# Performance work log

Hardware: AMD Instinct MI355X
Metric: run time of the kernel (lower is better)

## Reference

```python
import jax, jax.numpy as jnp
import numpy as np

N = 20000   # nodes
E = 320000  # edges (avg degree 16)
F = 8       # n_original_features (tokens per node)
D = 16      # embed_dim
H = 4       # num_heads
OUT = 7     # classes


def setup_inputs() -> dict:
    key = jax.random.key(0)
    ks = jax.random.split(key, 12)
    s = 0.1
    return {
        "x": jax.random.normal(ks[0], (N, F * D), dtype=jnp.float32),
        "edge_index": jax.random.randint(ks[1], (2, E), 0, N, dtype=jnp.int32),
        "conv1_wqkv": jax.random.normal(ks[2], (3 * D, D), dtype=jnp.float32) * s,
        "conv1_bqkv": jnp.zeros((3 * D,), dtype=jnp.float32),
        "conv1_wo": jax.random.normal(ks[3], (D, D), dtype=jnp.float32) * s,
        "conv1_bo": jnp.zeros((D,), dtype=jnp.float32),
        "conv2_wqkv": jax.random.normal(ks[4], (3 * D, D), dtype=jnp.float32) * s,
        "conv2_bqkv": jnp.zeros((3 * D,), dtype=jnp.float32),
        "conv2_wo": jax.random.normal(ks[5], (D, D), dtype=jnp.float32) * s,
        "conv2_bo": jnp.zeros((D,), dtype=jnp.float32),
        "out_w": jax.random.normal(ks[6], (OUT, F * D), dtype=jnp.float32) * s,
        "out_b": jnp.zeros((OUT,), dtype=jnp.float32),
    }


def _mha_edge(xq, xkv, wqkv, bqkv, wo, bo):
    # xq, xkv: [E, F, D]. torch MultiheadAttention: query=xq, key=value=xkv.
    dh = D // H
    wq, wk, wv = jnp.split(wqkv, 3, axis=0)
    bq, bk, bv = jnp.split(bqkv, 3)
    q = (xq @ wq.T + bq).reshape(-1, F, H, dh)
    k = (xkv @ wk.T + bk).reshape(-1, F, H, dh)
    v = (xkv @ wv.T + bv).reshape(-1, F, H, dh)
    scale = 1.0 / np.sqrt(dh).astype(np.float32)
    scores = jnp.einsum('efhd,eghd->ehfg', q, k) * scale  # [E,H,F,F]
    attn = jax.nn.softmax(scores, axis=-1)
    out = jnp.einsum('ehfg,eghd->efhd', attn, v).reshape(-1, F, D)
    return out @ wo.T + bo


def _amp_conv(x, src, dst, wqkv, bqkv, wo, bo):
    # gather per-edge token views; query = target node tokens (x_i), key/value = source (x_j)
    xj = x[src].reshape(-1, F, D)
    xi = x[dst].reshape(-1, F, D)
    msg = _mha_edge(xi, xj, wqkv, bqkv, wo, bo).reshape(-1, F * D)
    return jax.ops.segment_sum(msg, dst, num_segments=N)  # aggr='add' at targets


def reference(x, edge_index, conv1_wqkv, conv1_bqkv, conv1_wo, conv1_bo,
              conv2_wqkv, conv2_bqkv, conv2_wo, conv2_bo, out_w, out_b):
    src, dst = edge_index[0], edge_index[1]
    h = _amp_conv(x, src, dst, conv1_wqkv, conv1_bqkv, conv1_wo, conv1_bo)
    h = jax.nn.elu(h)
    h = _amp_conv(h, src, dst, conv2_wqkv, conv2_bqkv, conv2_wo, conv2_bo)
    h = jax.nn.elu(h)
    logits = h @ out_w.T + out_b
    return jax.nn.log_softmax(logits, axis=1)
```

## Files before the change

### kernel.cpp

```cpp
#include <hip/hip_runtime.h>
#include <hip/hip_bf16.h>
#include <math.h>

#define NN 20000
#define NE 320000
#define FT 8
#define DM 16
#define FD 128
#define OUTC 7
#define CHK 20
#define DEGB 1250

typedef unsigned short ushort;
typedef unsigned int uint;
typedef __fp16 h2 __attribute__((ext_vector_type(2)));
union UH { uint u; h2 h; };

__device__ inline h2 u2h(uint x) { UH c; c.u = x; return c.h; }

__device__ inline float dot2(uint a, h2 b, float c) {
#if __has_builtin(__builtin_amdgcn_fdot2)
    return __builtin_amdgcn_fdot2(u2h(a), b, c, false);
#else
    h2 ah = u2h(a);
    return fmaf((float)ah.x, (float)b.x, fmaf((float)ah.y, (float)b.y, c));
#endif
}
__device__ inline float dot2u(uint a, uint b, float c) { return dot2(a, u2h(b), c); }
__device__ inline float dot2h(h2 a, h2 b, float c) {
#if __has_builtin(__builtin_amdgcn_fdot2)
    return __builtin_amdgcn_fdot2(a, b, c, false);
#else
    return fmaf((float)a.x, (float)b.x, fmaf((float)a.y, (float)b.y, c));
#endif
}

__device__ inline h2 pk(float a, float b) {
#if __has_builtin(__builtin_amdgcn_cvt_pkrtz)
    return __builtin_amdgcn_cvt_pkrtz(a, b);
#else
    h2 r; r.x = (__fp16)a; r.y = (__fp16)b; return r;
#endif
}
__device__ inline ushort f16b(float x) {
    union { __fp16 h; ushort u; } c; c.h = (__fp16)x; return c.u;
}
__device__ inline float rcpf(float x) {
#if __has_builtin(__builtin_amdgcn_rcpf)
    return __builtin_amdgcn_rcpf(x);
#else
    return 1.0f / x;
#endif
}
__device__ inline float exp2r(float x) {
#if __has_builtin(__builtin_amdgcn_exp2f)
    return __builtin_amdgcn_exp2f(x);
#else
    return exp2f(x);
#endif
}
__device__ inline float elu_f(float x) {
    return x > 0.f ? x : exp2r(x * 1.4426950408889634f) - 1.0f;
}

__device__ inline void wave_lds_fence() { __threadfence_block(); }

#define QSCALE 0.7213475204444817f


__global__ __launch_bounds__(256) void qkv1_deg_kernel(
    const float* __restrict__ x,
    const float* __restrict__ wqkv, const float* __restrict__ bqkv,
    const int* __restrict__ dst, int* __restrict__ deg,
    ushort* __restrict__ qout, ushort* __restrict__ kvout) {
    if (blockIdx.x < DEGB) {
        const int e = blockIdx.x * 256 + threadIdx.x;
        if (e < NE) atomicAdd(&deg[dst[e]], 1);
        return;
    }
    __shared__ float sw[48 * 17];
    __shared__ float sb[48];
    __shared__ float sx[2][FD];
    __shared__ uint squ[2][64];
    __shared__ uint skvu[2][128];
    const int t = threadIdx.x;
    const int nh = t >> 7, tl = t & 127;
    const int nbase = (blockIdx.x - DEGB) * 4;
    for (int i = t; i < 48 * 16; i += 256) sw[(i >> 4) * 17 + (i & 15)] = wqkv[i];
    if (t < 48) sb[t] = bqkv[t];
    const int f = tl >> 4, d = tl & 15, h = d >> 2, dd = d & 3;
#pragma unroll
    for (int it = 0; it < 2; ++it) {
        const int n = nbase + it * 2 + nh;
        if (it) __syncthreads();
        sx[nh][tl] = x[(size_t)n * FD + tl];
        __syncthreads();
        float aq = sb[d], ak = sb[16 + d], av = sb[32 + d];
        const float* xr = &sx[nh][f * 16];
#pragma unroll
        for (int e = 0; e < 16; ++e) {
            const float xe = xr[e];
            aq = fmaf(xe, sw[d * 17 + e], aq);
            ak = fmaf(xe, sw[(16 + d) * 17 + e], ak);
            av = fmaf(xe, sw[(32 + d) * 17 + e], av);
        }
        ushort* sq = (ushort*)squ[nh];
        ushort* skv = (ushort*)skvu[nh];
        sq[tl] = f16b(aq * QSCALE);
        skv[h * 64 + f * 4 + dd] = f16b(ak);
        skv[h * 64 + 32 + dd * 8 + f] = f16b(av);
        __syncthreads();
        if (tl < 64) ((uint*)(qout + (size_t)n * FD))[tl] = squ[nh][tl];
        ((uint*)(kvout + (size_t)n * 256))[tl] = skvu[nh][tl];
    }
}

__global__ __launch_bounds__(1024) void scan_kernel(const int* __restrict__ deg,
                                                    int* __restrict__ rowstart,
                                                    int* __restrict__ cursor) {
    __shared__ int wsum[16];
    const int t = threadIdx.x;
    const int lane = t & 63, wid = t >> 6;
    const int base = t * CHK;
    int local[CHK];
    int s = 0;
#pragma unroll
    for (int i = 0; i < CHK; ++i) {
        const int idx = base + i;
        const int d = (idx < NN) ? deg[idx] : 0;
        local[i] = s;
        s += d;
    }
    int ws = s;
    for (int off = 1; off < 64; off <<= 1) {
        int tmp = __shfl_up(ws, off);
        if (lane >= off) ws += tmp;
    }
    if (lane == 63) wsum[wid] = ws;
    __syncthreads();
    if (wid == 0) {
        int v = (lane < 16) ? wsum[lane] : 0;
        for (int off = 1; off < 16; off <<= 1) {
            int tmp = __shfl_up(v, off);
            if (lane >= off) v += tmp;
        }
        if (lane < 16) wsum[lane] = v;
    }
    __syncthreads();
    const int excl = (ws - s) + (wid > 0 ? wsum[wid - 1] : 0);
#pragma unroll
    for (int i = 0; i < CHK; ++i) {
        const int idx = base + i;
        if (idx < NN) {
            const int v = excl + local[i];
            rowstart[idx] = v;
            cursor[idx] = v;
        }
    }
    if (t == 0) rowstart[NN] = NE;
}

__global__ __launch_bounds__(256) void scatter_kernel(
    const int* __restrict__ src, const int* __restrict__ dst,
    int* __restrict__ cursor, int* __restrict__ csr_src) {
    const int e = blockIdx.x * 256 + threadIdx.x;
    if (e < NE) {
        const int pos = atomicAdd(&cursor[dst[e]], 1);
        csr_src[pos] = src[e];
    }
}

template <int PHASE>
__global__ __launch_bounds__(256) void edge_fused_kernel(
    const int* __restrict__ rowstart, const int* __restrict__ csr_src,
    const ushort* __restrict__ qh, const uint* __restrict__ kvw,
    const float* __restrict__ wo, const float* __restrict__ bo,
    const float* __restrict__ w2, const float* __restrict__ b2,
    ushort* __restrict__ qout, ushort* __restrict__ kvout,
    float* __restrict__ out) {
    __shared__ float swb[1200];
    __shared__ float srow[4][FD];
    __shared__ uint spack[4][192];
    const int t = threadIdx.x;
    for (int i = t; i < 256; i += 256) swb[(i >> 4) * 17 + (i & 15)] = wo[i];
    if (t < 16) swb[272 + t] = bo[t];
    if (PHASE == 1) {
        for (int i = t; i < 768; i += 256) swb[288 + (i >> 4) * 17 + (i & 15)] = w2[i];
        if (t < 48) swb[1104 + t] = b2[t];
    } else {
        for (int i = t; i < OUTC * FD; i += 256) swb[288 + i] = w2[i];
        if (t < OUTC) swb[1184 + t] = b2[t];
    }
    __syncthreads();

    const int wv = t >> 6;
    const int n = blockIdx.x * 4 + wv;
    const int lane = t & 63;
    const int slot = lane >> 2, h = lane & 3;
    const h2 one2 = {(__fp16)1.0f, (__fp16)1.0f};

    const uint* qrow = (const uint*)(qh + (size_t)n * FD);
    uint2 qp[8];
#pragma unroll
    for (int f = 0; f < 8; ++f)
        qp[f] = *(const uint2*)(qrow + f * 8 + h * 2);

    const int beg = rowstart[n], end = rowstart[n + 1];

    float acc[8][4];
#pragma unroll
    for (int f = 0; f < 8; ++f)
#pragma unroll
        for (int dd = 0; dd < 4; ++dd) acc[f][dd] = 0.f;

    int e = beg + slot;
    uint idx = (e < end) ? (uint)csr_src[e] : 0u;
    float gate = (e < end) ? 1.0f : 0.0f;

    for (int eb = beg; eb < end; eb += 16) {
        const uint4* p = (const uint4*)(kvw + (size_t)idx * 128 + h * 32);
        const uint4 k0 = p[0], k1 = p[1], k2 = p[2], k3 = p[3];
        const uint4 v0 = p[4], v1 = p[5], v2 = p[6], v3 = p[7];
        const int en = eb + 16 + slot;
        const uint idxn = (en < end) ? (uint)csr_src[en] : 0u;
        const float gaten = (en < end) ? 1.0f : 0.0f;

#pragma unroll
        for (int f = 0; f < 8; ++f) {
            const uint qx = qp[f].x, qy = qp[f].y;
            float s0 = dot2u(qy, k0.y, dot2u(qx, k0.x, 0.f));
            float s1 = dot2u(qy, k0.w, dot2u(qx, k0.z, 0.f));
            float s2 = dot2u(qy, k1.y, dot2u(qx, k1.x, 0.f));
            float s3 = dot2u(qy, k1.w, dot2u(qx, k1.z, 0.f));
            float s4 = dot2u(qy, k2.y, dot2u(qx, k2.x, 0.f));
            float s5 = dot2u(qy, k2.w, dot2u(qx, k2.z, 0.f));
            float s6 = dot2u(qy, k3.y, dot2u(qx, k3.x, 0.f));
            float s7 = dot2u(qy, k3.w, dot2u(qx, k3.z, 0.f));
            s0 = exp2r(s0); s1 = exp2r(s1); s2 = exp2r(s2); s3 = exp2r(s3);
            s4 = exp2r(s4); s5 = exp2r(s5); s6 = exp2r(s6); s7 = exp2r(s7);
            const h2 e0 = pk(s0, s1), e1 = pk(s2, s3), e2 = pk(s4, s5), e3 = pk(s6, s7);
            const float sum =
                dot2h(e3, one2, dot2h(e2, one2, dot2h(e1, one2, dot2h(e0, one2, 0.f))));
            const float inv = gate * rcpf(sum);
            const float p0 = dot2(v0.w, e3, dot2(v0.z, e2, dot2(v0.y, e1, dot2(v0.x, e0, 0.f))));
            const float p1 = dot2(v1.w, e3, dot2(v1.z, e2, dot2(v1.y, e1, dot2(v1.x, e0, 0.f))));
            const float p2 = dot2(v2.w, e3, dot2(v2.z, e2, dot2(v2.y, e1, dot2(v2.x, e0, 0.f))));
            const float p3 = dot2(v3.w, e3, dot2(v3.z, e2, dot2(v3.y, e1, dot2(v3.x, e0, 0.f))));
            acc[f][0] = fmaf(p0, inv, acc[f][0]);
            acc[f][1] = fmaf(p1, inv, acc[f][1]);
            acc[f][2] = fmaf(p2, inv, acc[f][2]);
            acc[f][3] = fmaf(p3, inv, acc[f][3]);
        }
        idx = idxn; gate = gaten;
    }

#pragma unroll
    for (int f = 0; f < 8; ++f)
#pragma unroll
        for (int dd = 0; dd < 4; ++dd) {
            float a = acc[f][dd];
            a += __shfl_xor(a, 4);
            a += __shfl_xor(a, 8);
            a += __shfl_xor(a, 16);
            a += __shfl_xor(a, 32);
            acc[f][dd] = a;
        }
    if (slot == 0) {
#pragma unroll
        for (int f = 0; f < 8; ++f)
            *(float4*)(&srow[wv][f * 16 + h * 4]) =
                make_float4(acc[f][0], acc[f][1], acc[f][2], acc[f][3]);
    }
    wave_lds_fence();

    const int dgr = end - beg;
    const int f0 = lane >> 4, d = lane & 15;
    const float* swo = swb;
    const float* sbo = swb + 272;
    float hv0 = (float)dgr * sbo[d];
    float hv1 = hv0;
#pragma unroll
    for (int ee = 0; ee < 16; ++ee) {
        const float wde = swo[d * 17 + ee];
        hv0 = fmaf(srow[wv][f0 * 16 + ee], wde, hv0);
        hv1 = fmaf(srow[wv][(f0 + 4) * 16 + ee], wde, hv1);
    }
    hv0 = elu_f(hv0);
    hv1 = elu_f(hv1);

    if (PHASE == 1) {
        srow[wv][lane] = hv0;
        srow[wv][lane + 64] = hv1;
        wave_lds_fence();
        const float* swq = swb + 288;
        const float* sbq = swb + 1104;
        float aq0 = sbq[d], ak0 = sbq[16 + d], av0 = sbq[32 + d];
        float aq1 = aq0, ak1 = ak0, av1 = av0;
#pragma unroll
        for (int ee = 0; ee < 16; ++ee) {
            const float x0 = srow[wv][f0 * 16 + ee];
            const float x1 = srow[wv][(f0 + 4) * 16 + ee];
            const float wq = swq[d * 17 + ee];
            const float wk = swq[(16 + d) * 17 + ee];
            const float wvw = swq[(32 + d) * 17 + ee];
            aq0 = fmaf(x0, wq, aq0); aq1 = fmaf(x1, wq, aq1);
            ak0 = fmaf(x0, wk, ak0); ak1 = fmaf(x1, wk, ak1);
            av0 = fmaf(x0, wvw, av0); av1 = fmaf(x1, wvw, av1);
        }
        ushort* sq = (ushort*)&spack[wv][0];
        ushort* skv = (ushort*)&spack[wv][64];
        const int hh = d >> 2, dd = d & 3;
        sq[lane] = f16b(aq0 * QSCALE);
        sq[lane + 64] = f16b(aq1 * QSCALE);
        skv[hh * 64 + f0 * 4 + dd] = f16b(ak0);
        skv[hh * 64 + (f0 + 4) * 4 + dd] = f16b(ak1);
        skv[hh * 64 + 32 + dd * 8 + f0] = f16b(av0);
        skv[hh * 64 + 32 + dd * 8 + f0 + 4] = f16b(av1);
        wave_lds_fence();
        ((uint*)(qout + (size_t)n * FD))[lane] = spack[wv][lane];
        uint* kvo = (uint*)(kvout + (size_t)n * 256);
        kvo[lane] = spack[wv][64 + lane];
        kvo[lane + 64] = spack[wv][128 + lane];
    } else {
        const float* scw = swb + 288;
        const float* scb = swb + 1184;
        float p[OUTC];
#pragma unroll
        for (int c = 0; c < OUTC; ++c)
            p[c] = fmaf(hv0, scw[c * FD + lane], hv1 * scw[c * FD + lane + 64]);
#pragma unroll
        for (int c = 0; c < OUTC; ++c)
            for (int off = 32; off; off >>= 1) p[c] += __shfl_xor(p[c], off);
        if (lane == 0) {
            float lg[OUTC];
            float m = -1e30f;
#pragma unroll
            for (int c = 0; c < OUTC; ++c) { lg[c] = p[c] + scb[c]; m = fmaxf(m, lg[c]); }
            float s = 0.f;
#pragma unroll
            for (int c = 0; c < OUTC; ++c) s += __expf(lg[c] - m);
            const float lse = m + logf(s);
#pragma unroll
            for (int c = 0; c < OUTC; ++c) out[(size_t)n * OUTC + c] = lg[c] - lse;
        }
    }
}

extern "C" void kernel_launch(void* const* d_in, const int* in_sizes, int n_in,
                              void* d_out, int out_size, void* d_ws, size_t ws_size,
                              hipStream_t stream) {
    const float* x      = (const float*)d_in[0];
    const int*   ei     = (const int*)d_in[1];
    const float* w1qkv  = (const float*)d_in[2];
    const float* b1qkv  = (const float*)d_in[3];
    const float* w1o    = (const float*)d_in[4];
    const float* b1o    = (const float*)d_in[5];
    const float* w2qkv  = (const float*)d_in[6];
    const float* b2qkv  = (const float*)d_in[7];
    const float* w2o    = (const float*)d_in[8];
    const float* b2o    = (const float*)d_in[9];
    const float* outw   = (const float*)d_in[10];
    const float* outb   = (const float*)d_in[11];
    float* out = (float*)d_out;

    const int* srcp = ei;
    const int* dstp = ei + NE;

    ushort* qh    = (ushort*)d_ws;
    ushort* kvh   = qh + (size_t)NN * FD;
    ushort* qh2   = kvh + (size_t)NN * 256;
    ushort* kvh2  = qh2 + (size_t)NN * FD;
    int*    deg      = (int*)(kvh2 + (size_t)NN * 256);
    int*    rowstart = deg + NN;
    int*    cursor   = rowstart + NN + 1;
    int*    csr_src  = cursor + NN;

    (void)hipMemsetAsync(deg, 0, NN * sizeof(int), stream);
    qkv1_deg_kernel<<<DEGB + NN / 4, 256, 0, stream>>>(x, w1qkv, b1qkv, dstp, deg, qh, kvh);
    scan_kernel<<<1, 1024, 0, stream>>>(deg, rowstart, cursor);
    scatter_kernel<<<(NE + 255) / 256, 256, 0, stream>>>(srcp, dstp, cursor, csr_src);

    edge_fused_kernel<1><<<NN / 4, 256, 0, stream>>>(
        rowstart, csr_src, qh, (const uint*)kvh, w1o, b1o, w2qkv, b2qkv,
        qh2, kvh2, nullptr);
    edge_fused_kernel<2><<<NN / 4, 256, 0, stream>>>(
        rowstart, csr_src, qh2, (const uint*)kvh2, w2o, b2o, outw, outb,
        nullptr, nullptr, out);
}
```

Measured before the change: 204.7 us.

## Split each node's edge loop across two wavefronts and reduce through LDS

Each destination node is now handled by two wavefronts instead of one, each taking alternate chunks of 16 edges, and the grid doubles to NN/2 blocks. Partial accumulators are combined through a second shared-memory row after a block barrier, and the second wave exits early. The aim is to shorten the per-node serial edge loop (average degree 16, so about two chunks) and raise parallelism. The cost is more blocks that each reload weights into LDS, an added __syncthreads, and half the waves sitting idle during the epilogue.

```diff
diff --git a/kernel.cpp b/kernel.cpp
--- a/kernel.cpp
+++ b/kernel.cpp
@@ -179,8 +179,9 @@
     ushort* __restrict__ qout, ushort* __restrict__ kvout,
     float* __restrict__ out) {
     __shared__ float swb[1200];
-    __shared__ float srow[4][FD];
-    __shared__ uint spack[4][192];
+    __shared__ float srow[2][FD];
+    __shared__ float srow2[2][FD];
+    __shared__ uint spack[2][192];
     const int t = threadIdx.x;
     for (int i = t; i < 256; i += 256) swb[(i >> 4) * 17 + (i & 15)] = wo[i];
     if (t < 16) swb[272 + t] = bo[t];
@@ -193,8 +194,10 @@
     }
     __syncthreads();
 
-    const int wv = t >> 6;
-    const int n = blockIdx.x * 4 + wv;
+    const int w4 = t >> 6;
+    const int nh = w4 >> 1;
+    const int ww = w4 & 1;
+    const int n = blockIdx.x * 2 + nh;
     const int lane = t & 63;
     const int slot = lane >> 2, h = lane & 3;
     const h2 one2 = {(__fp16)1.0f, (__fp16)1.0f};
@@ -213,15 +216,16 @@
 #pragma unroll
         for (int dd = 0; dd < 4; ++dd) acc[f][dd] = 0.f;
 
-    int e = beg + slot;
+    const int wbeg = beg + ww * 16;
+    int e = wbeg + slot;
     uint idx = (e < end) ? (uint)csr_src[e] : 0u;
     float gate = (e < end) ? 1.0f : 0.0f;
 
-    for (int eb = beg; eb < end; eb += 16) {
+    for (int eb = wbeg; eb < end; eb += 32) {
         const uint4* p = (const uint4*)(kvw + (size_t)idx * 128 + h * 32);
         const uint4 k0 = p[0], k1 = p[1], k2 = p[2], k3 = p[3];
         const uint4 v0 = p[4], v1 = p[5], v2 = p[6], v3 = p[7];
-        const int en = eb + 16 + slot;
+        const int en = eb + 32 + slot;
         const uint idxn = (en < end) ? (uint)csr_src[en] : 0u;
         const float gaten = (en < end) ? 1.0f : 0.0f;
 
@@ -266,11 +270,17 @@
             acc[f][dd] = a;
         }
     if (slot == 0) {
+        float* dstrow = (ww == 0) ? srow[nh] : srow2[nh];
 #pragma unroll
         for (int f = 0; f < 8; ++f)
-            *(float4*)(&srow[wv][f * 16 + h * 4]) =
+            *(float4*)(&dstrow[f * 16 + h * 4]) =
                 make_float4(acc[f][0], acc[f][1], acc[f][2], acc[f][3]);
     }
+    __syncthreads();
+    if (ww == 1) return;
+
+    srow[nh][lane] += srow2[nh][lane];
+    srow[nh][lane + 64] += srow2[nh][lane + 64];
     wave_lds_fence();
 
     const int dgr = end - beg;
@@ -282,15 +292,15 @@
 #pragma unroll
     for (int ee = 0; ee < 16; ++ee) {
         const float wde = swo[d * 17 + ee];
-        hv0 = fmaf(srow[wv][f0 * 16 + ee], wde, hv0);
-        hv1 = fmaf(srow[wv][(f0 + 4) * 16 + ee], wde, hv1);
+        hv0 = fmaf(srow[nh][f0 * 16 + ee], wde, hv0);
+        hv1 = fmaf(srow[nh][(f0 + 4) * 16 + ee], wde, hv1);
     }
     hv0 = elu_f(hv0);
     hv1 = elu_f(hv1);
 
     if (PHASE == 1) {
-        srow[wv][lane] = hv0;
-        srow[wv][lane + 64] = hv1;
+        srow[nh][lane] = hv0;
+        srow[nh][lane + 64] = hv1;
         wave_lds_fence();
         const float* swq = swb + 288;
         const float* sbq = swb + 1104;
@@ -298,8 +308,8 @@
         float aq1 = aq0, ak1 = ak0, av1 = av0;
 #pragma unroll
         for (int ee = 0; ee < 16; ++ee) {
-            const float x0 = srow[wv][f0 * 16 + ee];
-            const float x1 = srow[wv][(f0 + 4) * 16 + ee];
+            const float x0 = srow[nh][f0 * 16 + ee];
+            const float x1 = srow[nh][(f0 + 4) * 16 + ee];
             const float wq = swq[d * 17 + ee];
             const float wk = swq[(16 + d) * 17 + ee];
             const float wvw = swq[(32 + d) * 17 + ee];
@@ -307,8 +317,8 @@
             ak0 = fmaf(x0, wk, ak0); ak1 = fmaf(x1, wk, ak1);
             av0 = fmaf(x0, wvw, av0); av1 = fmaf(x1, wvw, av1);
         }
-        ushort* sq = (ushort*)&spack[wv][0];
-        ushort* skv = (ushort*)&spack[wv][64];
+        ushort* sq = (ushort*)&spack[nh][0];
+        ushort* skv = (ushort*)&spack[nh][64];
         const int hh = d >> 2, dd = d & 3;
         sq[lane] = f16b(aq0 * QSCALE);
         sq[lane + 64] = f16b(aq1 * QSCALE);
@@ -317,10 +327,10 @@
         skv[hh * 64 + 32 + dd * 8 + f0] = f16b(av0);
         skv[hh * 64 + 32 + dd * 8 + f0 + 4] = f16b(av1);
         wave_lds_fence();
-        ((uint*)(qout + (size_t)n * FD))[lane] = spack[wv][lane];
+        ((uint*)(qout + (size_t)n * FD))[lane] = spack[nh][lane];
         uint* kvo = (uint*)(kvout + (size_t)n * 256);
-        kvo[lane] = spack[wv][64 + lane];
-        kvo[lane + 64] = spack[wv][128 + lane];
+        kvo[lane] = spack[nh][64 + lane];
+        kvo[lane + 64] = spack[nh][128 + lane];
     } else {
         const float* scw = swb + 288;
         const float* scb = swb + 1184;
@@ -380,10 +390,10 @@
     scan_kernel<<<1, 1024, 0, stream>>>(deg, rowstart, cursor);
     scatter_kernel<<<(NE + 255) / 256, 256, 0, stream>>>(srcp, dstp, cursor, csr_src);
 
-    edge_fused_kernel<1><<<NN / 4, 256, 0, stream>>>(
+    edge_fused_kernel<1><<<NN / 2, 256, 0, stream>>>(
         rowstart, csr_src, qh, (const uint*)kvh, w1o, b1o, w2qkv, b2qkv,
         qh2, kvh2, nullptr);
-    edge_fused_kernel<2><<<NN / 4, 256, 0, stream>>>(
+    edge_fused_kernel<2><<<NN / 2, 256, 0, stream>>>(
         rowstart, csr_src, qh2, (const uint*)kvh2, w2o, b2o, outw, outb,
         nullptr, nullptr, out);
 }
```

Result: slower. 258.1 us (+26.1%).
